# Performance work log

Hardware: AMD Instinct MI355X
Metric: run time of the kernel (lower is better)

The kernel has to match this reference:

```python
import jax, jax.numpy as jnp
import numpy as np

NSAMPLE = 64
RADIUS = 0.3
HMIN = -0.2
HMAX_LIST = (0.1, 0.2, 0.3, 0.4)
NUM_ANGLE = 12
NUM_DEPTH = 4
EPS = 1e-5


def setup_inputs() -> dict:
    key = jax.random.key(0)
    ks = jax.random.split(key, 32)
    rn = lambda i, s: jax.random.normal(ks[i], s, dtype=jnp.float32)
    ru = lambda i, s: jax.random.uniform(ks[i], s, dtype=jnp.float32)
    return {
        'seed_xyz': rn(0, (2, 1024, 3)),
        'pointcloud': rn(1, (2, 8192, 3)),
        'vp_rot': rn(2, (2, 1024, 3, 3)),
        'cw1': rn(3, (64, 3)), 'cbn1': ru(4, (4, 64)),
        'cw2': rn(5, (128, 64)), 'cbn2': ru(6, (4, 128)),
        'cw3': rn(7, (256, 128)), 'cbn3': ru(8, (4, 256)),
        'ow1': rn(9, (128, 256)), 'ob1': rn(10, (128,)), 'obn1': ru(11, (4, 128)),
        'ow2': rn(12, (128, 128)), 'ob2': rn(13, (128,)), 'obn2': ru(14, (4, 128)),
        'ow3': rn(15, (36, 128)), 'ob3': rn(16, (36,)),
        'tw1': rn(17, (128, 256)), 'tb1': rn(18, (128,)), 'tbn1': ru(19, (4, 128)),
        'tw2': rn(20, (128, 128)), 'tb2': rn(21, (128,)), 'tbn2': ru(22, (4, 128)),
        'tw3': rn(23, (12, 128)), 'tb3': rn(24, (12,)),
    }


def _bn_relu(y, bn):
    g, b, m, v = bn[0], bn[1], bn[2], bn[3]
    return jax.nn.relu(g * (y - m) * jax.lax.rsqrt(v + EPS) + b)


def _bn(y, bn):
    g, b, m, v = bn[0], bn[1], bn[2], bn[3]
    return g * (y - m) * jax.lax.rsqrt(v + EPS) + b


def _forward(seed_xyz, pointcloud, vp_rot, cw1, cbn1, cw2, cbn2, cw3, cbn3,
             ow1, ob1, obn1, ow2, ob2, obn2, ow3, ob3,
             tw1, tb1, tbn1, tw2, tb2, tbn2, tw3, tb3):
    B, ns, _ = seed_xyz.shape
    N = pointcloud.shape[1]
    # relative coords of every scene point w.r.t. every seed, rotated into the
    # grasp-view frame (cylinder axis = x after rotation): (B, ns, N, 3)
    rel = pointcloud[:, None, :, :] - seed_xyz[:, :, None, :]
    rot_rel = jnp.einsum('bsnc,bscd->bsnd', rel, vp_rot)
    ax = rot_rel[..., 0]
    r2 = rot_rel[..., 1] ** 2 + rot_rel[..., 2] ** 2
    pref = jnp.arange(N, dtype=jnp.float32) / N  # earlier index preferred (CUDA scan order)
    groups = []
    for hmax in HMAX_LIST:
        mask = (ax > HMIN) & (ax < hmax) & (r2 < RADIUS * RADIUS)
        score = mask.astype(jnp.float32) * 2.0 - pref
        _, idx = jax.lax.top_k(score, NSAMPLE)  # (B, ns, NSAMPLE), first valid idxs in order
        valid = jnp.take_along_axis(mask, idx, axis=-1)
        idx = jnp.where(valid, idx, idx[..., :1])  # fill slots with first found index
        g = jnp.take_along_axis(rot_rel, idx[..., None], axis=2)  # (B, ns, NSAMPLE, 3)
        groups.append(g)
    feat = jnp.stack(groups, axis=2)  # (B, ns, num_depth, NSAMPLE, 3)
    feat = feat.reshape(B, ns * NUM_DEPTH, NSAMPLE, 3)
    # SharedMLP [3,64,128,256], conv2d 1x1 (no bias) + BN + ReLU
    h = _bn_relu(feat @ cw1.T, cbn1)
    h = _bn_relu(h @ cw2.T, cbn2)
    h = _bn_relu(h @ cw3.T, cbn3)
    vp = jnp.max(h, axis=2)  # max-pool over nsample -> (B, ns*num_depth, 256)

    def head(w1, b1, bn1, w2, b2, bn2, w3, b3):
        x = _bn_relu(vp @ w1.T + b1, bn1)
        x = _bn_relu(x @ w2.T + b2, bn2)
        return x @ w3.T + b3

    op = head(ow1, ob1, obn1, ow2, ob2, obn2, ow3, ob3)     # (B, ns*D, 3*num_angle)
    tol = head(tw1, tb1, tbn1, tw2, tb2, tbn2, tw3, tb3)    # (B, ns*D, num_angle)
    out = jnp.concatenate([op, tol], axis=-1)               # score|angle_cls|width|tolerance
    out = out.reshape(B, ns, NUM_DEPTH, 4 * NUM_ANGLE).transpose(0, 3, 1, 2)
    return out  # (B, 4*num_angle, num_seed, num_depth)


def reference(seed_xyz, pointcloud, vp_rot, cw1, cbn1, cw2, cbn2, cw3, cbn3,
              ow1, ob1, obn1, ow2, ob2, obn2, ow3, ob3,
              tw1, tb1, tbn1, tw2, tb2, tbn2, tw3, tb3):
    return _forward(seed_xyz, pointcloud, vp_rot, cw1, cbn1, cw2, cbn2, cw3, cbn3,
                    ow1, ob1, obn1, ow2, ob2, obn2, ow3, ob3,
                    tw1, tb1, tbn1, tw2, tb2, tbn2, tw3, tb3)
```

## Files before the change

kernel.cpp:

```cpp
#include <hip/hip_runtime.h>
#include <hip/hip_bf16.h>

#define NB    2
#define NS    1024
#define NPTS  8192
#define NGROUP (NB*NS*4)

enum : int {
  OFF_BW2  = 256,
  OFF_W1Q  = 4352,
  OFF_B2   = 8448,
  OFF_BW3  = 8576,
  OFF_B3   = 41344,
  OFF_HB1  = 41600,
  OFF_HB1B = 74368,
  OFF_HB2  = 74624,
  OFF_HB2B = 107392,
  OFF_HB3  = 107648,
  OFF_HB3B = 115840,
  OFF_FEAT = 146688,
  OFF_VP   = 1719552,
  OFF_PCX  = 1719552,
  OFF_PCY  = 1735936,
  OFF_PCZ  = 1752320,
  OFF_SEED = 1768704,
  OFF_ROT  = 1774848,
  OFF_CNT  = 3816704,
  OFF_FLAG = 3824896,
  PREP_TOTAL = 189632 + 6144 + 18432 + 49152,
};

struct Ptrs { const void* p[25]; };

typedef __attribute__((ext_vector_type(8))) short bf16x8;
typedef __attribute__((ext_vector_type(4))) float f32x4;

template<typename T> struct LD;
template<> struct LD<float> {
  static __device__ __forceinline__ float get(const void* p, int i){ return ((const float*)p)[i]; }
};
template<> struct LD<__hip_bfloat16> {
  static __device__ __forceinline__ float get(const void* p, int i){ return __bfloat162float(((const __hip_bfloat16*)p)[i]); }
};

template<typename T>
__device__ __forceinline__ float bnscale(const void* bn, int C, int c){
  float g = LD<T>::get(bn, c);
  float v = LD<T>::get(bn, 3*C + c);
  return g / sqrtf(v + 1e-5f);
}

__device__ __forceinline__ unsigned short f2bf(float v){
  __hip_bfloat16 hb = __float2bfloat16(v);
  return *reinterpret_cast<unsigned short*>(&hb);
}

__global__ __launch_bounds__(256) void detect_kernel(const void* w2, const void* w3, int* flag){
  __shared__ int f;
  int t = threadIdx.x;
  if (t == 0) f = 0;
  __syncthreads();
  int loc = 0;
  auto chk = [&](unsigned u){
    loc |= ((u & 0x7F80u) == 0x7F80u);
    loc |= (((u >> 16) & 0x7F80u) == 0x7F80u);
  };
  const uint4* a = (const uint4*)w2;
  for (int i = t; i < 1024; i += 256) { uint4 u = a[i]; chk(u.x); chk(u.y); chk(u.z); chk(u.w); }
  const uint4* b = (const uint4*)w3;
  for (int i = t; i < 4096; i += 256) { uint4 u = b[i]; chk(u.x); chk(u.y); chk(u.z); chk(u.w); }
  if (loc) atomicOr(&f, 1);
  __syncthreads();
  if (t == 0) flag[0] = f;
}

template<typename T>
__device__ void prep_body(const Ptrs& in, float* __restrict__ ws, int i){
  if (i < 256) { int c = i>>2, d = i&3; float s = bnscale<T>(in.p[4],64,c);
    float v = (d<3) ? LD<T>::get(in.p[3], c*3+d)*s
                    : LD<T>::get(in.p[4],64+c) - LD<T>::get(in.p[4],2*64+c)*s;
    ws[OFF_W1Q+i] = v; return; }
  i -= 256;
  if (i < 8192) {
    int j = i&7, f = i>>3, lane = f&63, kn = f>>6, kt = kn&1, nt = kn>>1;
    int n = nt*16 + (lane&15), k = kt*32 + ((lane>>4)<<3) + j;
    float s = bnscale<T>(in.p[6],128,n);
    ((unsigned short*)(ws + OFF_BW2))[i] = f2bf(LD<T>::get(in.p[5], n*64+k)*s); return; }
  i -= 8192;
  if (i < 32768) {
    int j = i&7, f = i>>3, lane = f&63, kn = f>>6, kt = kn&3, nt = kn>>2;
    int n = nt*16 + (lane&15), k = kt*32 + ((lane>>4)<<3) + j;
    float s = bnscale<T>(in.p[8],256,n);
    ((unsigned short*)(ws + OFF_BW3))[i] = f2bf(LD<T>::get(in.p[7], n*128+k)*s); return; }
  i -= 32768;
  if (i < 128) { float s = bnscale<T>(in.p[6],128,i);
    ws[OFF_B2+i] = LD<T>::get(in.p[6],128+i) - LD<T>::get(in.p[6],2*128+i)*s; return; }
  i -= 128;
  if (i < 256) { float s = bnscale<T>(in.p[8],256,i);
    ws[OFF_B3+i] = LD<T>::get(in.p[8],256+i) - LD<T>::get(in.p[8],2*256+i)*s; return; }
  i -= 256;
  if (i < 65536) {
    int j = i&7, f = i>>3, lane = f&63, kn = f>>6, kt = kn&7, nt = kn>>3;
    int n = nt*16 + (lane&15), k = kt*32 + ((lane>>4)<<3) + j;
    float v;
    if (n < 128) v = LD<T>::get(in.p[9],  n*256+k)       * bnscale<T>(in.p[11],128,n);
    else         v = LD<T>::get(in.p[17], (n-128)*256+k) * bnscale<T>(in.p[19],128,n-128);
    ((unsigned short*)(ws + OFF_HB1))[i] = f2bf(v); return; }
  i -= 65536;
  if (i < 256) { int n = i; float v;
    if (n < 128) { float s = bnscale<T>(in.p[11],128,n);
      v = (LD<T>::get(in.p[10],n) - LD<T>::get(in.p[11],2*128+n))*s + LD<T>::get(in.p[11],128+n); }
    else { int m = n-128; float s = bnscale<T>(in.p[19],128,m);
      v = (LD<T>::get(in.p[18],m) - LD<T>::get(in.p[19],2*128+m))*s + LD<T>::get(in.p[19],128+m); }
    ws[OFF_HB1B+n] = v; return; }
  i -= 256;
  if (i < 65536) {
    int j = i&7, f = i>>3, lane = f&63, kn = f>>6, kt = kn&7, nt = kn>>3;
    int n = nt*16 + (lane&15), k = kt*32 + ((lane>>4)<<3) + j;
    float v = 0.f;
    if (n < 128) { if (k < 128)  v = LD<T>::get(in.p[12], n*128+k)            * bnscale<T>(in.p[14],128,n); }
    else         { if (k >= 128) v = LD<T>::get(in.p[20], (n-128)*128+(k-128)) * bnscale<T>(in.p[22],128,n-128); }
    ((unsigned short*)(ws + OFF_HB2))[i] = f2bf(v); return; }
  i -= 65536;
  if (i < 256) { int n = i; float v;
    if (n < 128) { float s = bnscale<T>(in.p[14],128,n);
      v = (LD<T>::get(in.p[13],n) - LD<T>::get(in.p[14],2*128+n))*s + LD<T>::get(in.p[14],128+n); }
    else { int m = n-128; float s = bnscale<T>(in.p[22],128,m);
      v = (LD<T>::get(in.p[21],m) - LD<T>::get(in.p[22],2*128+m))*s + LD<T>::get(in.p[22],128+m); }
    ws[OFF_HB2B+n] = v; return; }
  i -= 256;
  if (i < 16384) {
    int j = i&7, f = i>>3, lane = f&63, kn = f>>6, kt = kn&7, nt = kn>>3;
    int n = nt*16 + (lane&15), k = kt*32 + ((lane>>4)<<3) + j;
    float v = 0.f;
    if (n < 36)      { if (k < 128)  v = LD<T>::get(in.p[15], n*128+k); }
    else if (n < 48) { if (k >= 128) v = LD<T>::get(in.p[23], (n-36)*128+(k-128)); }
    ((unsigned short*)(ws + OFF_HB3))[i] = f2bf(v); return; }
  i -= 16384;
  if (i < 64) { int n = i; float v = 0.f;
    if (n < 36) v = LD<T>::get(in.p[16], n);
    else if (n < 48) v = LD<T>::get(in.p[24], n-36);
    ws[OFF_HB3B+n] = v; return; }
  i -= 64;
  if (i < 6144)  { ws[OFF_SEED+i] = LD<T>::get(in.p[0], i); return; }
  i -= 6144;
  if (i < 18432) { ws[OFF_ROT+i] = LD<T>::get(in.p[2], i); return; }
  i -= 18432;
  {
    int arr = i >> 14, idx = i & 16383;
    ws[OFF_PCX + arr*16384 + idx] = LD<T>::get(in.p[1], idx*3 + arr); }
}

__global__ __launch_bounds__(256) void prep_kernel(Ptrs in, float* __restrict__ ws){
  int i = blockIdx.x*256 + threadIdx.x;
  if (i >= PREP_TOTAL) return;
  if (((const volatile int*)(ws + OFF_FLAG))[0]) prep_body<float>(in, ws, i);
  else                                           prep_body<__hip_bfloat16>(in, ws, i);
}

__global__ __launch_bounds__(256) void group_kernel(float* __restrict__ ws){
#pragma clang fp contract(off)
  __shared__ float scratch[2][2][4][192];
  __shared__ int   cl[2][2][4];
  __shared__ float p0s[2][3];
  const int t = threadIdx.x;
  const int wave = t >> 6, lane = t & 63;
  const int s = wave >> 1, half = wave & 1;
  const int seedIdx = blockIdx.x*2 + s;
  const int b = seedIdx >> 10;
  const float sx = ws[OFF_SEED + seedIdx*3+0];
  const float sy = ws[OFF_SEED + seedIdx*3+1];
  const float sz = ws[OFF_SEED + seedIdx*3+2];
  const float r00=ws[OFF_ROT+seedIdx*9+0], r01=ws[OFF_ROT+seedIdx*9+1], r02=ws[OFF_ROT+seedIdx*9+2];
  const float r10=ws[OFF_ROT+seedIdx*9+3], r11=ws[OFF_ROT+seedIdx*9+4], r12=ws[OFF_ROT+seedIdx*9+5];
  const float r20=ws[OFF_ROT+seedIdx*9+6], r21=ws[OFF_ROT+seedIdx*9+7], r22=ws[OFF_ROT+seedIdx*9+8];
  const float* px = ws + OFF_PCX + b*8192;
  const float* py = ws + OFF_PCY + b*8192;
  const float* pz = ws + OFF_PCZ + b*8192;
  if (half == 0 && lane == 0) {
    float e0 = px[0] - sx, e1 = py[0] - sy, e2 = pz[0] - sz;
    p0s[s][0] = e0*r00 + e1*r10 + e2*r20;
    p0s[s][1] = e0*r01 + e1*r11 + e2*r21;
    p0s[s][2] = e0*r02 + e1*r12 + e2*r22;
  }
  float* s0 = scratch[s][half][0];
  float* s1 = scratch[s][half][1];
  float* s2 = scratch[s][half][2];
  float* s3 = scratch[s][half][3];
  int c0n=0, c1n=0, c2n=0, c3n=0;
  const int basept = half*4096;
  const unsigned long long pm = (1ull << lane) - 1ull;

  auto scan = [&](float x, float y, float z){
    float e0 = x - sx, e1 = y - sy, e2 = z - sz;
    float rx = e0*r00 + e1*r10 + e2*r20;
    float ry = e0*r01 + e1*r11 + e2*r21;
    float rz = e0*r02 + e1*r12 + e2*r22;
    float r2 = ry*ry + rz*rz;
    const bool mb = (rx > -0.2f) && (r2 < 0.09f);
    { bool m = mb && (rx < 0.1f); unsigned long long bal = __ballot(m);
      if (bal) { int slot = c0n + __popcll(bal & pm);
        if (m && slot < 64) { s0[slot*3]=rx; s0[slot*3+1]=ry; s0[slot*3+2]=rz; }
        c0n += __popcll(bal); } }
    { bool m = mb && (rx < 0.2f); unsigned long long bal = __ballot(m);
      if (bal) { int slot = c1n + __popcll(bal & pm);
        if (m && slot < 64) { s1[slot*3]=rx; s1[slot*3+1]=ry; s1[slot*3+2]=rz; }
        c1n += __popcll(bal); } }
    { bool m = mb && (rx < 0.3f); unsigned long long bal = __ballot(m);
      if (bal) { int slot = c2n + __popcll(bal & pm);
        if (m && slot < 64) { s2[slot*3]=rx; s2[slot*3+1]=ry; s2[slot*3+2]=rz; }
        c2n += __popcll(bal); } }
    { bool m = mb && (rx < 0.4f); unsigned long long bal = __ballot(m);
      if (bal) { int slot = c3n + __popcll(bal & pm);
        if (m && slot < 64) { s3[slot*3]=rx; s3[slot*3+1]=ry; s3[slot*3+2]=rz; }
        c3n += __popcll(bal); } }
  };

  for (int c = 0; c < 64; c += 2) {
    const int i0 = basept + c*64 + lane;
    float xA = px[i0],    yA = py[i0],    zA = pz[i0];
    float xB = px[i0+64], yB = py[i0+64], zB = pz[i0+64];
    scan(xA, yA, zA);
    scan(xB, yB, zB);
  }
  if (lane == 0) { cl[s][half][0]=c0n; cl[s][half][1]=c1n; cl[s][half][2]=c2n; cl[s][half][3]=c3n; }
  __syncthreads();
  for (int idx = t; idx < 512; idx += 256) {
    const int ss = idx >> 8, rem = idx & 255, bin = rem >> 6, slot = rem & 63;
    int ca = cl[ss][0][bin]; if (ca > 64) ca = 64;
    int cb = cl[ss][1][bin];
    const int g = (blockIdx.x*2 + ss)*4 + bin;
    float* fo = ws + OFF_FEAT + g*192;
    if (slot < ca) {
      fo[slot*3+0] = scratch[ss][0][bin][slot*3+0];
      fo[slot*3+1] = scratch[ss][0][bin][slot*3+1];
      fo[slot*3+2] = scratch[ss][0][bin][slot*3+2];
    }
    int nb = 64 - ca; if (cb < nb) nb = cb;
    if (slot < nb) {
      fo[(ca+slot)*3+0] = scratch[ss][1][bin][slot*3+0];
      fo[(ca+slot)*3+1] = scratch[ss][1][bin][slot*3+1];
      fo[(ca+slot)*3+2] = scratch[ss][1][bin][slot*3+2];
    }
  }
  if (t < 8) {
    const int ss = t >> 2, bin = t & 3;
    int tot = cl[ss][0][bin] + cl[ss][1][bin]; if (tot > 64) tot = 64;
    const int g = (blockIdx.x*2 + ss)*4 + bin;
    float* fo = ws + OFF_FEAT + g*192;
    if (tot == 0) { fo[0]=p0s[ss][0]; fo[1]=p0s[ss][1]; fo[2]=p0s[ss][2]; tot = 1; }
    ((int*)(ws + OFF_CNT))[g] = tot;
  }
}

__global__ __launch_bounds__(256) void mlp_kernel(float* __restrict__ ws){
  __shared__ unsigned short h2s[2][64*136];
  __shared__ float w1q[4][256];
  const int t = threadIdx.x;
  const int wave = t >> 6, lane = t & 63;
  const int quad = lane >> 4, l15 = lane & 15;
  const int grp = wave >> 1, nhalf = wave & 1;
  const int g = blockIdx.x*2 + grp;
  for (int i = t; i < 1024; i += 256) w1q[i>>8][i&255] = ws[OFF_W1Q + (i&255)];
  const int V = ((const int*)(ws + OFF_CNT))[g];
  const float* feat = ws + OFF_FEAT + g*192;
  __syncthreads();
  bf16x8 a1[4][2];
  const float* wq = w1q[quad];
#pragma unroll
  for (int mt = 0; mt < 4; ++mt) {
    const int m = mt*16 + l15;
    const float x0 = feat[m*3+0], x1 = feat[m*3+1], x2 = feat[m*3+2];
#pragma unroll
    for (int kt = 0; kt < 2; ++kt) {
      const int c0 = kt*32 + quad*8;
#pragma unroll
      for (int j = 0; j < 8; ++j) {
        const float* w = wq + (c0+j)*4;
        a1[mt][kt][j] = (short)f2bf(fmaxf(w[3] + x0*w[0] + x1*w[1] + x2*w[2], 0.f));
      }
    }
  }
  unsigned short* h2 = h2s[grp];
  const bf16x8* BW2 = (const bf16x8*)(ws + OFF_BW2);
#pragma unroll
  for (int nt4 = 0; nt4 < 4; ++nt4) {
    const int nt = nhalf*4 + nt4;
    const int n = nt*16 + l15;
    const float bias = ws[OFF_B2 + n];
    f32x4 acc[4];
#pragma unroll
    for (int mt = 0; mt < 4; ++mt) acc[mt] = (f32x4){bias, bias, bias, bias};
#pragma unroll
    for (int kt = 0; kt < 2; ++kt) {
      const bf16x8 b = BW2[(nt*2+kt)*64 + lane];
#pragma unroll
      for (int mt = 0; mt < 4; ++mt)
        acc[mt] = __builtin_amdgcn_mfma_f32_16x16x32_bf16(a1[mt][kt], b, acc[mt], 0, 0, 0);
    }
#pragma unroll
    for (int mt = 0; mt < 4; ++mt)
#pragma unroll
      for (int jj = 0; jj < 4; ++jj) {
        const int m = mt*16 + quad*4 + jj;
        h2[m*136 + n] = f2bf(fmaxf(acc[mt][jj], 0.f));
      }
  }
  __syncthreads();
  bf16x8 a2[4][4];
#pragma unroll
  for (int mt = 0; mt < 4; ++mt)
#pragma unroll
    for (int kt = 0; kt < 4; ++kt)
      a2[mt][kt] = *(const bf16x8*)&h2[(mt*16 + l15)*136 + kt*32 + quad*8];
  const bf16x8* BW3 = (const bf16x8*)(ws + OFF_BW3);
  float vpv[8];
#pragma unroll
  for (int nt8 = 0; nt8 < 8; ++nt8) {
    const int nt = nhalf*8 + nt8;
    const int n = nt*16 + l15;
    const float bias = ws[OFF_B3 + n];
    f32x4 acc[4];
#pragma unroll
    for (int mt = 0; mt < 4; ++mt) acc[mt] = (f32x4){bias, bias, bias, bias};
#pragma unroll
    for (int kt = 0; kt < 4; ++kt) {
      const bf16x8 b = BW3[(nt*4+kt)*64 + lane];
#pragma unroll
      for (int mt = 0; mt < 4; ++mt)
        acc[mt] = __builtin_amdgcn_mfma_f32_16x16x32_bf16(a2[mt][kt], b, acc[mt], 0, 0, 0);
    }
    float mx = 0.f;
#pragma unroll
    for (int mt = 0; mt < 4; ++mt)
#pragma unroll
      for (int jj = 0; jj < 4; ++jj) {
        const int row = mt*16 + quad*4 + jj;
        const float v = fmaxf(acc[mt][jj], 0.f);
        mx = (row < V) ? fmaxf(mx, v) : mx;
      }
    mx = fmaxf(mx, __shfl_xor(mx, 16, 64));
    mx = fmaxf(mx, __shfl_xor(mx, 32, 64));
    vpv[nt8] = mx;
  }
  if (quad == 0) {
    float* vp = ws + OFF_VP + g*256 + nhalf*128;
#pragma unroll
    for (int nt8 = 0; nt8 < 8; ++nt8) vp[nt8*16 + l15] = vpv[nt8];
  }
}

#define YSTRIDE 264
__global__ __launch_bounds__(256) void heads_kernel(float* __restrict__ ws, void* __restrict__ outv){
  const int isf32 = ((const volatile int*)(ws + OFF_FLAG))[0];
  __shared__ unsigned short y[16*YSTRIDE];
  const int t = threadIdx.x;
  const int wave = t >> 6, lane = t & 63;
  const int quad = lane >> 4, l15 = lane & 15;
  const int r0 = blockIdx.x * 16;
  bf16x8 a[8];
  const float* vp = ws + OFF_VP + (r0 + l15)*256;
#pragma unroll
  for (int kt = 0; kt < 8; ++kt) {
    const float4* v4 = (const float4*)(vp + kt*32 + quad*8);
    float4 u0 = v4[0], u1 = v4[1];
    a[kt][0]=(short)f2bf(u0.x); a[kt][1]=(short)f2bf(u0.y); a[kt][2]=(short)f2bf(u0.z); a[kt][3]=(short)f2bf(u0.w);
    a[kt][4]=(short)f2bf(u1.x); a[kt][5]=(short)f2bf(u1.y); a[kt][6]=(short)f2bf(u1.z); a[kt][7]=(short)f2bf(u1.w);
  }
  const bf16x8* HB1 = (const bf16x8*)(ws + OFF_HB1);
#pragma unroll
  for (int nt4 = 0; nt4 < 4; ++nt4) {
    const int nt = wave*4 + nt4;
    const int n = nt*16 + l15;
    const float bias = ws[OFF_HB1B + n];
    f32x4 acc = (f32x4){bias, bias, bias, bias};
#pragma unroll
    for (int kt = 0; kt < 8; ++kt)
      acc = __builtin_amdgcn_mfma_f32_16x16x32_bf16(a[kt], HB1[(nt*8+kt)*64 + lane], acc, 0, 0, 0);
#pragma unroll
    for (int jj = 0; jj < 4; ++jj)
      y[(quad*4+jj)*YSTRIDE + n] = f2bf(fmaxf(acc[jj], 0.f));
  }
  __syncthreads();
#pragma unroll
  for (int kt = 0; kt < 8; ++kt)
    a[kt] = *(const bf16x8*)&y[l15*YSTRIDE + kt*32 + quad*8];
  __syncthreads();
  const bf16x8* HB2 = (const bf16x8*)(ws + OFF_HB2);
#pragma unroll
  for (int nt4 = 0; nt4 < 4; ++nt4) {
    const int nt = wave*4 + nt4;
    const int n = nt*16 + l15;
    const float bias = ws[OFF_HB2B + n];
    f32x4 acc = (f32x4){bias, bias, bias, bias};
#pragma unroll
    for (int kt = 0; kt < 8; ++kt)
      acc = __builtin_amdgcn_mfma_f32_16x16x32_bf16(a[kt], HB2[(nt*8+kt)*64 + lane], acc, 0, 0, 0);
#pragma unroll
    for (int jj = 0; jj < 4; ++jj)
      y[(quad*4+jj)*YSTRIDE + n] = f2bf(fmaxf(acc[jj], 0.f));
  }
  __syncthreads();
#pragma unroll
  for (int kt = 0; kt < 8; ++kt)
    a[kt] = *(const bf16x8*)&y[l15*YSTRIDE + kt*32 + quad*8];
  const bf16x8* HB3 = (const bf16x8*)(ws + OFF_HB3);
  {
    const int n = wave*16 + l15;
    const float bias = ws[OFF_HB3B + n];
    f32x4 acc = (f32x4){bias, bias, bias, bias};
#pragma unroll
    for (int kt = 0; kt < 8; ++kt)
      acc = __builtin_amdgcn_mfma_f32_16x16x32_bf16(a[kt], HB3[(wave*8+kt)*64 + lane], acc, 0, 0, 0);
    if (n < 48) {
#pragma unroll
      for (int jj = 0; jj < 4; ++jj) {
        const int gr = r0 + quad*4 + jj;
        const int b = gr >> 12, rem = gr & 4095, s = rem >> 2, d = rem & 3;
        const int o = ((b*48 + n)*1024 + s)*4 + d;
        if (isf32) ((float*)outv)[o] = acc[jj];
        else       ((__hip_bfloat16*)outv)[o] = __float2bfloat16(acc[jj]);
      }
    }
  }
}

extern "C" void kernel_launch(void* const* d_in, const int* in_sizes, int n_in,
                              void* d_out, int out_size, void* d_ws, size_t ws_size,
                              hipStream_t stream) {
  float* ws = (float*)d_ws;
  Ptrs P;
  for (int i = 0; i < 25; ++i) P.p[i] = d_in[i];
  detect_kernel<<<1, 256, 0, stream>>>(d_in[5], d_in[7], (int*)(ws + OFF_FLAG));
  prep_kernel<<<(PREP_TOTAL+255)/256, 256, 0, stream>>>(P, ws);
  group_kernel<<<NB*NS/2, 256, 0, stream>>>(ws);
  mlp_kernel<<<NGROUP/2, 256, 0, stream>>>(ws);
  heads_kernel<<<NGROUP/16, 256, 0, stream>>>(ws, d_out);
}
```

Baseline: 216.4 us.

## Fold dtype detection into prep, pad groups with duplicates, transpose layer-2 MFMA

Removes the separate dtype-detect launch by having every prep block scan w3 itself and derive the float/bf16 flag locally. The group kernel now fills all 64 slots, padding with a duplicate valid point (or the fallback point), so the per-group count buffer and the row<V masking in the MLP max-pool go away. The second MLP layer swaps the MFMA operands so weights are the A operand, which allows vectorised bias loads and packed bf16 stores into LDS. In exchange every prep block redundantly reads w3, and the detection only checks w3 rather than both weight tensors.

```diff
diff --git a/kernel.cpp b/kernel.cpp
--- a/kernel.cpp
+++ b/kernel.cpp
@@ -25,7 +25,6 @@
   OFF_PCZ  = 1752320,
   OFF_SEED = 1768704,
   OFF_ROT  = 1774848,
-  OFF_CNT  = 3816704,
   OFF_FLAG = 3824896,
   PREP_TOTAL = 189632 + 6144 + 18432 + 49152,
 };
@@ -55,24 +54,17 @@
   return *reinterpret_cast<unsigned short*>(&hb);
 }
 
-__global__ __launch_bounds__(256) void detect_kernel(const void* w2, const void* w3, int* flag){
-  __shared__ int f;
-  int t = threadIdx.x;
-  if (t == 0) f = 0;
-  __syncthreads();
-  int loc = 0;
-  auto chk = [&](unsigned u){
-    loc |= ((u & 0x7F80u) == 0x7F80u);
-    loc |= (((u >> 16) & 0x7F80u) == 0x7F80u);
-  };
-  const uint4* a = (const uint4*)w2;
-  for (int i = t; i < 1024; i += 256) { uint4 u = a[i]; chk(u.x); chk(u.y); chk(u.z); chk(u.w); }
-  const uint4* b = (const uint4*)w3;
-  for (int i = t; i < 4096; i += 256) { uint4 u = b[i]; chk(u.x); chk(u.y); chk(u.z); chk(u.w); }
-  if (loc) atomicOr(&f, 1);
-  __syncthreads();
-  if (t == 0) flag[0] = f;
-}
+#if __has_builtin(__builtin_amdgcn_cvt_pk_bf16_f32)
+typedef __attribute__((ext_vector_type(2))) __bf16 bf16x2_t;
+__device__ __forceinline__ unsigned pk2bf(float a, float b){
+  bf16x2_t r = __builtin_amdgcn_cvt_pk_bf16_f32(a, b);
+  return *reinterpret_cast<unsigned*>(&r);
+}
+#else
+__device__ __forceinline__ unsigned pk2bf(float a, float b){
+  return (unsigned)f2bf(a) | ((unsigned)f2bf(b) << 16);
+}
+#endif
 
 template<typename T>
 __device__ void prep_body(const Ptrs& in, float* __restrict__ ws, int i){
@@ -152,10 +144,28 @@
 }
 
 __global__ __launch_bounds__(256) void prep_kernel(Ptrs in, float* __restrict__ ws){
-  int i = blockIdx.x*256 + threadIdx.x;
+  __shared__ int sf;
+  const int t = threadIdx.x;
+  if (t == 0) sf = 0;
+  __syncthreads();
+  int loc = 0;
+  const uint4* w3r = (const uint4*)in.p[7];
+#pragma unroll
+  for (int k = 0; k < 8; ++k) {
+    uint4 u = w3r[t + k*256];
+    loc |= ((u.x & 0x7F80u) == 0x7F80u) | (((u.x>>16) & 0x7F80u) == 0x7F80u);
+    loc |= ((u.y & 0x7F80u) == 0x7F80u) | (((u.y>>16) & 0x7F80u) == 0x7F80u);
+    loc |= ((u.z & 0x7F80u) == 0x7F80u) | (((u.z>>16) & 0x7F80u) == 0x7F80u);
+    loc |= ((u.w & 0x7F80u) == 0x7F80u) | (((u.w>>16) & 0x7F80u) == 0x7F80u);
+  }
+  if (loc) atomicOr(&sf, 1);
+  __syncthreads();
+  const int isf32 = sf;
+  const int i = blockIdx.x*256 + t;
+  if (i == 0) ((int*)(ws + OFF_FLAG))[0] = isf32;
   if (i >= PREP_TOTAL) return;
-  if (((const volatile int*)(ws + OFF_FLAG))[0]) prep_body<float>(in, ws, i);
-  else                                           prep_body<__hip_bfloat16>(in, ws, i);
+  if (isf32) prep_body<float>(in, ws, i);
+  else       prep_body<__hip_bfloat16>(in, ws, i);
 }
 
 __global__ __launch_bounds__(256) void group_kernel(float* __restrict__ ws){
@@ -226,30 +236,20 @@
   if (lane == 0) { cl[s][half][0]=c0n; cl[s][half][1]=c1n; cl[s][half][2]=c2n; cl[s][half][3]=c3n; }
   __syncthreads();
   for (int idx = t; idx < 512; idx += 256) {
-    const int ss = idx >> 8, rem = idx & 255, bin = rem >> 6, slot = rem & 63;
+    const int ss = idx >> 8, bin = (idx >> 6) & 3, slot = idx & 63;
     int ca = cl[ss][0][bin]; if (ca > 64) ca = 64;
     int cb = cl[ss][1][bin];
+    const float* A = scratch[ss][0][bin];
+    const float* B = scratch[ss][1][bin];
+    float fx, fy, fz;
+    if (slot < ca)              { fx=A[slot*3]; fy=A[slot*3+1]; fz=A[slot*3+2]; }
+    else if (slot - ca < cb)    { int q = slot-ca; fx=B[q*3]; fy=B[q*3+1]; fz=B[q*3+2]; }
+    else if (ca > 0)            { fx=A[0]; fy=A[1]; fz=A[2]; }
+    else if (cb > 0)            { fx=B[0]; fy=B[1]; fz=B[2]; }
+    else                        { fx=p0s[ss][0]; fy=p0s[ss][1]; fz=p0s[ss][2]; }
     const int g = (blockIdx.x*2 + ss)*4 + bin;
     float* fo = ws + OFF_FEAT + g*192;
-    if (slot < ca) {
-      fo[slot*3+0] = scratch[ss][0][bin][slot*3+0];
-      fo[slot*3+1] = scratch[ss][0][bin][slot*3+1];
-      fo[slot*3+2] = scratch[ss][0][bin][slot*3+2];
-    }
-    int nb = 64 - ca; if (cb < nb) nb = cb;
-    if (slot < nb) {
-      fo[(ca+slot)*3+0] = scratch[ss][1][bin][slot*3+0];
-      fo[(ca+slot)*3+1] = scratch[ss][1][bin][slot*3+1];
-      fo[(ca+slot)*3+2] = scratch[ss][1][bin][slot*3+2];
-    }
-  }
-  if (t < 8) {
-    const int ss = t >> 2, bin = t & 3;
-    int tot = cl[ss][0][bin] + cl[ss][1][bin]; if (tot > 64) tot = 64;
-    const int g = (blockIdx.x*2 + ss)*4 + bin;
-    float* fo = ws + OFF_FEAT + g*192;
-    if (tot == 0) { fo[0]=p0s[ss][0]; fo[1]=p0s[ss][1]; fo[2]=p0s[ss][2]; tot = 1; }
-    ((int*)(ws + OFF_CNT))[g] = tot;
+    fo[slot*3+0]=fx; fo[slot*3+1]=fy; fo[slot*3+2]=fz;
   }
 }
 
@@ -262,49 +262,47 @@
   const int grp = wave >> 1, nhalf = wave & 1;
   const int g = blockIdx.x*2 + grp;
   for (int i = t; i < 1024; i += 256) w1q[i>>8][i&255] = ws[OFF_W1Q + (i&255)];
-  const int V = ((const int*)(ws + OFF_CNT))[g];
   const float* feat = ws + OFF_FEAT + g*192;
   __syncthreads();
-  bf16x8 a1[4][2];
+  bf16x8 b1[4][2];
   const float* wq = w1q[quad];
 #pragma unroll
-  for (int mt = 0; mt < 4; ++mt) {
-    const int m = mt*16 + l15;
-    const float x0 = feat[m*3+0], x1 = feat[m*3+1], x2 = feat[m*3+2];
+  for (int Nt = 0; Nt < 4; ++Nt) {
+    const int sm = Nt*16 + l15;
+    const float x0 = feat[sm*3+0], x1 = feat[sm*3+1], x2 = feat[sm*3+2];
 #pragma unroll
     for (int kt = 0; kt < 2; ++kt) {
       const int c0 = kt*32 + quad*8;
 #pragma unroll
       for (int j = 0; j < 8; ++j) {
         const float* w = wq + (c0+j)*4;
-        a1[mt][kt][j] = (short)f2bf(fmaxf(w[3] + x0*w[0] + x1*w[1] + x2*w[2], 0.f));
+        b1[Nt][kt][j] = (short)f2bf(fmaxf(w[3] + x0*w[0] + x1*w[1] + x2*w[2], 0.f));
       }
     }
   }
   unsigned short* h2 = h2s[grp];
   const bf16x8* BW2 = (const bf16x8*)(ws + OFF_BW2);
 #pragma unroll
-  for (int nt4 = 0; nt4 < 4; ++nt4) {
-    const int nt = nhalf*4 + nt4;
-    const int n = nt*16 + l15;
-    const float bias = ws[OFF_B2 + n];
+  for (int mt4 = 0; mt4 < 4; ++mt4) {
+    const int Mt = nhalf*4 + mt4;
+    const f32x4 bias4 = *(const f32x4*)(ws + OFF_B2 + Mt*16 + quad*4);
     f32x4 acc[4];
 #pragma unroll
-    for (int mt = 0; mt < 4; ++mt) acc[mt] = (f32x4){bias, bias, bias, bias};
+    for (int Nt = 0; Nt < 4; ++Nt) acc[Nt] = bias4;
 #pragma unroll
     for (int kt = 0; kt < 2; ++kt) {
-      const bf16x8 b = BW2[(nt*2+kt)*64 + lane];
-#pragma unroll
-      for (int mt = 0; mt < 4; ++mt)
-        acc[mt] = __builtin_amdgcn_mfma_f32_16x16x32_bf16(a1[mt][kt], b, acc[mt], 0, 0, 0);
-    }
-#pragma unroll
-    for (int mt = 0; mt < 4; ++mt)
-#pragma unroll
-      for (int jj = 0; jj < 4; ++jj) {
-        const int m = mt*16 + quad*4 + jj;
-        h2[m*136 + n] = f2bf(fmaxf(acc[mt][jj], 0.f));
-      }
+      const bf16x8 aw = BW2[(Mt*2+kt)*64 + lane];
+#pragma unroll
+      for (int Nt = 0; Nt < 4; ++Nt)
+        acc[Nt] = __builtin_amdgcn_mfma_f32_16x16x32_bf16(aw, b1[Nt][kt], acc[Nt], 0, 0, 0);
+    }
+#pragma unroll
+    for (int Nt = 0; Nt < 4; ++Nt) {
+      const unsigned lo = pk2bf(fmaxf(acc[Nt][0],0.f), fmaxf(acc[Nt][1],0.f));
+      const unsigned hi = pk2bf(fmaxf(acc[Nt][2],0.f), fmaxf(acc[Nt][3],0.f));
+      uint2* dst = (uint2*)&h2[(Nt*16 + l15)*136 + Mt*16 + quad*4];
+      *dst = make_uint2(lo, hi);
+    }
   }
   __syncthreads();
   bf16x8 a2[4][4];
@@ -332,13 +330,10 @@
     }
     float mx = 0.f;
 #pragma unroll
-    for (int mt = 0; mt < 4; ++mt)
-#pragma unroll
-      for (int jj = 0; jj < 4; ++jj) {
-        const int row = mt*16 + quad*4 + jj;
-        const float v = fmaxf(acc[mt][jj], 0.f);
-        mx = (row < V) ? fmaxf(mx, v) : mx;
-      }
+    for (int mt = 0; mt < 4; ++mt) {
+      mx = fmaxf(mx, fmaxf(fmaxf(acc[mt][0], acc[mt][1]), fmaxf(acc[mt][2], acc[mt][3])));
+    }
+    mx = fmaxf(mx, 0.f);
     mx = fmaxf(mx, __shfl_xor(mx, 16, 64));
     mx = fmaxf(mx, __shfl_xor(mx, 32, 64));
     vpv[nt8] = mx;
@@ -431,7 +426,6 @@
   float* ws = (float*)d_ws;
   Ptrs P;
   for (int i = 0; i < 25; ++i) P.p[i] = d_in[i];
-  detect_kernel<<<1, 256, 0, stream>>>(d_in[5], d_in[7], (int*)(ws + OFF_FLAG));
   prep_kernel<<<(PREP_TOTAL+255)/256, 256, 0, stream>>>(P, ws);
   group_kernel<<<NB*NS/2, 256, 0, stream>>>(ws);
   mlp_kernel<<<NGROUP/2, 256, 0, stream>>>(ws);
```

Result: faster. 210.5 us (-2.7%).
